# Performance work log

Hardware: AMD Instinct MI355X
Metric: run time of the kernel (lower is better)

## Reference

```python
import jax, jax.numpy as jnp
import numpy as np

N, C, NUM_ELL, E = 1024, 128, 16, 10          # nodes, channels, sum(2l+1) for lmax=3, num_elements
OUT_IRREPS = [(0, 1), (1, 3)]                  # (l_out, 2*l_out+1) for target 128x0e + 128x1o
CORRELATION = 3
NPATHS = {3: 11, 2: 4, 1: 1}                   # generalized-CG path counts per correlation order


def setup_inputs() -> dict:
    key = jax.random.key(0)
    ks = jax.random.split(key, 40)
    node_feats = jax.random.normal(ks[0], (N, C, NUM_ELL), dtype=jnp.float32)
    elem = jax.random.randint(ks[1], (N,), 0, E)
    node_attrs = jax.nn.one_hot(elem, E, dtype=jnp.float32)           # one-hot element indicator
    out_dim = C * sum(d for _, d in OUT_IRREPS)                        # 512
    sc = jax.random.normal(ks[2], (N, out_dim), dtype=jnp.float32)
    inp = {"node_feats": node_feats, "sc": sc, "node_attrs": node_attrs}
    i = 3
    for li, (_, d) in enumerate(OUT_IRREPS):
        for nu in range(1, CORRELATION + 1):
            k = NPATHS[nu]
            # U_nu: generalized CG tensor, shape [d_out, num_ell^nu ..., n_paths]
            inp[f"U_{li}_{nu}"] = jax.random.normal(ks[i], (d,) + (NUM_ELL,) * nu + (k,), dtype=jnp.float32) * np.float32(0.1)
            i += 1
            # element-indexed path weights [num_elements, n_paths, channels]
            inp[f"W_{li}_{nu}"] = jax.random.normal(ks[i], (E, k, C), dtype=jnp.float32) * np.float32(1.0 / np.sqrt(k * C))
            i += 1
        # e3nn-style per-irrep linear mixing multiplicities [C, C]
        inp[f"lin_{li}"] = jax.random.normal(ks[i], (C, C), dtype=jnp.float32)
        i += 1
    return inp


def _sym_contraction(x, y, U, W):
    # x: [N, C, num_ell], y: [N, E]; MACE Contraction recursion (highest order first)
    nu = CORRELATION
    wb = jnp.einsum("ekc,be->bkc", W[nu], y)                 # gather per-element weights
    out = jnp.einsum("...ik,bkc,bci->bc...", U[nu], wb, x)   # [N, C, d, ell, ell] for nu=3
    for nu in range(CORRELATION - 1, 0, -1):
        wb = jnp.einsum("ekc,be->bkc", W[nu], y)
        c = jnp.einsum("...k,bkc->bc...", U[nu], wb) + out
        out = jnp.einsum("bc...i,bci->bc...", c, x)          # contract one ell axis per step
    return out                                               # [N, C, d_out]


def reference(node_feats, sc, node_attrs,
              U_0_1, U_0_2, U_0_3, W_0_1, W_0_2, W_0_3, lin_0,
              U_1_1, U_1_2, U_1_3, W_1_1, W_1_2, W_1_3, lin_1):
    Us = [{1: U_0_1, 2: U_0_2, 3: U_0_3}, {1: U_1_1, 2: U_1_2, 3: U_1_3}]
    Ws = [{1: W_0_1, 2: W_0_2, 3: W_0_3}, {1: W_1_1, 2: W_1_2, 3: W_1_3}]
    lins = [lin_0, lin_1]
    inv_sqrt_c = np.float32(1.0 / np.sqrt(C))                # e3nn Linear fan-in normalization
    blocks = []
    for li in range(len(OUT_IRREPS)):
        feats = _sym_contraction(node_feats, node_attrs, Us[li], Ws[li])   # [N, C, d]
        lin_out = jnp.einsum("bcd,cf->bfd", feats, lins[li]) * inv_sqrt_c
        blocks.append(lin_out.reshape(node_feats.shape[0], -1))           # mul_ir flatten [N, C*d]
    return jnp.concatenate(blocks, axis=-1) + sc             # residual self-connection
```

## Files before the change

### kernel.cpp

```cpp
#include <hip/hip_runtime.h>

#define N_NODES 1024
#define C_CH    128
#define N_ELEM  10
#define K3      11
#define W3PM    1040
#define SU2OFF  49920

__global__ __launch_bounds__(256) void precompute_kernel(
    const float* __restrict__ U03, const float* __restrict__ U02,
    const float* __restrict__ U13, const float* __restrict__ U12,
    float* __restrict__ ws)
{
  const int t = blockIdx.x * 256 + threadIdx.x;
  if (t < 4160) {
    const int m = t / W3PM;
    const int j = t - m * W3PM;
    int a = 0, b = 0, off = 0;
    bool fnd = false;
    for (a = 0; a < 16 && !fnd; ++a) {
      for (b = 0; b <= a; ++b) {
        const int rl = ((b >> 2) + 1) << 2;
        if (j < off + rl) { fnd = true; break; }
        off += rl;
      }
      if (fnd) break;
    }
    const int cc = j - off;
    float out[12];
    #pragma unroll
    for (int k = 0; k < 12; ++k) out[k] = 0.f;
    if (cc <= b) {
      const float* U3 = (m == 0) ? U03 : (U13 + (size_t)(m - 1) * 45056);
      int bases[6]; int np = 0;
      if (a == b && b == cc) {
        bases[np++] = ((a * 16 + a) * 16 + a) * K3;
      } else if (a == b) {
        bases[np++] = ((a * 16 + a) * 16 + cc) * K3;
        bases[np++] = ((a * 16 + cc) * 16 + a) * K3;
        bases[np++] = ((cc * 16 + a) * 16 + a) * K3;
      } else if (b == cc) {
        bases[np++] = ((a * 16 + b) * 16 + b) * K3;
        bases[np++] = ((b * 16 + a) * 16 + b) * K3;
        bases[np++] = ((b * 16 + b) * 16 + a) * K3;
      } else {
        bases[np++] = ((a * 16 + b) * 16 + cc) * K3;
        bases[np++] = ((a * 16 + cc) * 16 + b) * K3;
        bases[np++] = ((b * 16 + a) * 16 + cc) * K3;
        bases[np++] = ((b * 16 + cc) * 16 + a) * K3;
        bases[np++] = ((cc * 16 + a) * 16 + b) * K3;
        bases[np++] = ((cc * 16 + b) * 16 + a) * K3;
      }
      for (int p = 0; p < np; ++p) {
        const float* src = U3 + bases[p];
        #pragma unroll
        for (int k = 0; k < K3; ++k) out[k] += src[k];
      }
    }
    float* dst = ws + (size_t)t * 12;
    *(float4*)&dst[0] = make_float4(out[0], out[1], out[2],  out[3]);
    *(float4*)&dst[4] = make_float4(out[4], out[5], out[6],  out[7]);
    *(float4*)&dst[8] = make_float4(out[8], out[9], out[10], out[11]);
  } else if (t < 4704) {
    const int u = t - 4160;
    const int m = u / 136;
    const int q = u - m * 136;
    int a = 0, b = q;
    while (b > a) { b -= (a + 1); ++a; }
    const float* U2 = (m == 0) ? U02 : (U12 + (size_t)(m - 1) * 1024);
    const float* p1 = U2 + (a * 16 + b) * 4;
    float4 r = make_float4(p1[0], p1[1], p1[2], p1[3]);
    if (a != b) {
      const float* p2 = U2 + (b * 16 + a) * 4;
      r.x += p2[0]; r.y += p2[1]; r.z += p2[2]; r.w += p2[3];
    }
    ((float4*)(ws + SU2OFF))[u] = r;
  }
}

__global__ __launch_bounds__(256) void sym_contract_kernel(
    const float* __restrict__ node_feats,
    const float* __restrict__ node_attrs,
    const float* __restrict__ W03, const float* __restrict__ W02,
    const float* __restrict__ W01, const float* __restrict__ W13,
    const float* __restrict__ W12, const float* __restrict__ W11,
    const float* __restrict__ U01, const float* __restrict__ U11,
    const float* __restrict__ ws,
    float* __restrict__ feats_out)
{
  __shared__ float W3c[4 * W3PM];
  __shared__ float T2c[4 * 136];
  __shared__ float T1s[64];
  __shared__ unsigned short nodelist[N_NODES];
  __shared__ float wrow[32];
  __shared__ int cnt;

  const int e   = blockIdx.x / C_CH;
  const int c   = blockIdx.x % C_CH;
  const int tid = threadIdx.x;

  if (tid == 0) cnt = 0;
  if (tid < 32) {
    float v;
    if (tid < 11)       v = W03[(e * K3 + tid) * C_CH + c];
    else if (tid < 15)  v = W02[(e * 4 + (tid - 11)) * C_CH + c];
    else if (tid == 15) v = W01[e * C_CH + c];
    else if (tid < 27)  v = W13[(e * K3 + (tid - 16)) * C_CH + c];
    else if (tid < 31)  v = W12[(e * 4 + (tid - 27)) * C_CH + c];
    else                v = W11[e * C_CH + c];
    wrow[tid] = v;
  }
  __syncthreads();

  for (int nd = tid; nd < N_NODES; nd += 256)
    if (node_attrs[nd * N_ELEM + e] > 0.5f)
      nodelist[atomicAdd(&cnt, 1)] = (unsigned short)nd;

  for (int ms = 0; ms < 4; ++ms) {
    const int wb = (ms == 0) ? 0 : 16;
    const float w0 = wrow[wb],     w1 = wrow[wb + 1], w2 = wrow[wb + 2];
    const float w3 = wrow[wb + 3], w4 = wrow[wb + 4], w5 = wrow[wb + 5];
    const float w6 = wrow[wb + 6], w7 = wrow[wb + 7], w8 = wrow[wb + 8];
    const float w9 = wrow[wb + 9], wA = wrow[wb + 10];
    for (int j = tid; j < W3PM; j += 256) {
      const float* r = ws + ((size_t)ms * W3PM + j) * 12;
      const float4 r0 = *(const float4*)&r[0];
      const float4 r1 = *(const float4*)&r[4];
      const float4 r2 = *(const float4*)&r[8];
      float acc =       r0.x * w0;
      acc = fmaf(r0.y, w1, acc); acc = fmaf(r0.z, w2, acc);
      acc = fmaf(r0.w, w3, acc); acc = fmaf(r1.x, w4, acc);
      acc = fmaf(r1.y, w5, acc); acc = fmaf(r1.z, w6, acc);
      acc = fmaf(r1.w, w7, acc); acc = fmaf(r2.x, w8, acc);
      acc = fmaf(r2.y, w9, acc); acc = fmaf(r2.z, wA, acc);
      W3c[ms * W3PM + j] = acc;
    }
  }
  const float4* SU2 = (const float4*)(ws + SU2OFF);
  for (int ms = 0; ms < 4; ++ms) {
    const int wb = (ms == 0) ? 11 : 27;
    const float q0 = wrow[wb], q1 = wrow[wb + 1], q2 = wrow[wb + 2], q3 = wrow[wb + 3];
    for (int q = tid; q < 136; q += 256) {
      const float4 r = SU2[ms * 136 + q];
      float acc = r.x * q0;
      acc = fmaf(r.y, q1, acc); acc = fmaf(r.z, q2, acc); acc = fmaf(r.w, q3, acc);
      T2c[ms * 136 + q] = acc;
    }
  }
  if (tid < 64) {
    const int mm = tid >> 4, i1 = tid & 15;
    T1s[tid] = (mm == 0) ? U01[i1] * wrow[15] : U11[(mm - 1) * 16 + i1] * wrow[31];
  }
  __syncthreads();

  const int m    = tid >> 6;
  const int lane = tid & 63;
  const float* W3m = W3c + m * W3PM;
  const float* T2m = T2c + m * 136;
  const float* T1m = T1s + m * 16;
  const int total = cnt;

  for (int base = 0; base < total; base += 64) {
    const int idx     = base + lane;
    const bool active = idx < total;
    const int nd = nodelist[active ? idx : 0];
    const float* xr = node_feats + ((size_t)nd * C_CH + c) * 16;
    float xs[16];
    *(float4*)&xs[0]  = ((const float4*)xr)[0];
    *(float4*)&xs[4]  = ((const float4*)xr)[1];
    *(float4*)&xs[8]  = ((const float4*)xr)[2];
    *(float4*)&xs[12] = ((const float4*)xr)[3];

    float acc0 = 0.f, acc1 = 0.f;
    int woff = 0, tp = 0;
    #pragma unroll
    for (int a = 0; a < 16; ++a) {
      float i1a = T1m[a], i1b = 0.f;
      #pragma unroll
      for (int b = 0; b <= a; ++b) {
        float in2 = T2m[tp];
        #pragma unroll
        for (int q = 0; q <= (b >> 2); ++q) {
          const float4 w4 = *(const float4*)&W3m[woff + 4 * q];
          in2 = fmaf(w4.x, xs[4 * q + 0], in2);
          in2 = fmaf(w4.y, xs[4 * q + 1], in2);
          in2 = fmaf(w4.z, xs[4 * q + 2], in2);
          in2 = fmaf(w4.w, xs[4 * q + 3], in2);
        }
        if (b & 1) i1b = fmaf(in2, xs[b], i1b);
        else       i1a = fmaf(in2, xs[b], i1a);
        woff += ((b >> 2) + 1) << 2;
        ++tp;
      }
      const float in1 = i1a + i1b;
      if (a & 1) acc1 = fmaf(in1, xs[a], acc1);
      else       acc0 = fmaf(in1, xs[a], acc0);
    }
    if (active)
      feats_out[(size_t)nd * 512 + c * 4 + m] = acc0 + acc1;
  }
}

__global__ __launch_bounds__(256) void linear_kernel(
    const float* __restrict__ sc,
    const float* __restrict__ lin0,
    const float* __restrict__ lin1,
    float* __restrict__ io)
{
  __shared__ float f[512];
  const int b   = blockIdx.x;
  const int tid = threadIdx.x;
  const float* row = io + (size_t)b * 512;
  if (tid < 128) ((float4*)f)[tid] = ((const float4*)row)[tid];
  __syncthreads();
  const float inv_sqrt_c = 0.088388347648318447f;
  #pragma unroll
  for (int rep = 0; rep < 2; ++rep) {
    const int o = tid + rep * 256;
    float acc = 0.f;
    if (o < 128) {
      const int fo = o;
      #pragma unroll 4
      for (int ci = 0; ci < 128; ++ci) acc = fmaf(f[ci * 4], lin0[ci * 128 + fo], acc);
    } else {
      const int oo = o - 128;
      const int fo = oo / 3;
      const int dd = oo - fo * 3;
      #pragma unroll 4
      for (int ci = 0; ci < 128; ++ci) acc = fmaf(f[ci * 4 + 1 + dd], lin1[ci * 128 + fo], acc);
    }
    io[(size_t)b * 512 + o] = fmaf(acc, inv_sqrt_c, sc[(size_t)b * 512 + o]);
  }
}

extern "C" void kernel_launch(void* const* d_in, const int* in_sizes, int n_in,
                              void* d_out, int out_size, void* d_ws, size_t ws_size,
                              hipStream_t stream) {
  const float* node_feats = (const float*)d_in[0];
  const float* sc         = (const float*)d_in[1];
  const float* node_attrs = (const float*)d_in[2];
  const float* U01  = (const float*)d_in[3];
  const float* W01  = (const float*)d_in[4];
  const float* U02  = (const float*)d_in[5];
  const float* W02  = (const float*)d_in[6];
  const float* U03  = (const float*)d_in[7];
  const float* W03  = (const float*)d_in[8];
  const float* lin0 = (const float*)d_in[9];
  const float* U11  = (const float*)d_in[10];
  const float* W11  = (const float*)d_in[11];
  const float* U12  = (const float*)d_in[12];
  const float* W12  = (const float*)d_in[13];
  const float* U13  = (const float*)d_in[14];
  const float* W13  = (const float*)d_in[15];
  const float* lin1 = (const float*)d_in[16];
  float* out = (float*)d_out;
  float* ws  = (float*)d_ws;

  precompute_kernel<<<19, 256, 0, stream>>>(U03, U02, U13, U12, ws);
  sym_contract_kernel<<<N_ELEM * C_CH, 256, 0, stream>>>(
      node_feats, node_attrs,
      W03, W02, W01, W13, W12, W11, U01, U11, ws, out);
  linear_kernel<<<N_NODES, 256, 0, stream>>>(sc, lin0, lin1, out);
}
```

Before: 142.1 us.

## Split per-(element,channel) weight table build into separate kernel read from global

Moves the per-block construction of the contracted U·W tables out of the contraction kernel into a dedicated table kernel that writes them to a workspace in global memory. The contraction kernel then reads weights straight from global (uniform scalar loads via readfirstlane) instead of shared memory, which drops the large shared allocation and may raise occupancy. The cost is an extra kernel launch plus about 24 MB of table writes and reads. The path only runs if the workspace is large enough, otherwise it falls back to the old kernel.

```diff
diff --git a/kernel.cpp b/kernel.cpp
--- a/kernel.cpp
+++ b/kernel.cpp
@@ -6,6 +6,8 @@
 #define K3      11
 #define W3PM    1040
 #define SU2OFF  49920
+#define TABOFF  52096
+#define TABSTR  4800
 
 __global__ __launch_bounds__(256) void precompute_kernel(
     const float* __restrict__ U03, const float* __restrict__ U02,
@@ -78,6 +80,146 @@
   }
 }
 
+__device__ __forceinline__ void build_wrow(
+    int e, int c, int tid, float* wrow,
+    const float* W03, const float* W02, const float* W01,
+    const float* W13, const float* W12, const float* W11)
+{
+  if (tid < 32) {
+    float v;
+    if (tid < 11)       v = W03[(e * K3 + tid) * C_CH + c];
+    else if (tid < 15)  v = W02[(e * 4 + (tid - 11)) * C_CH + c];
+    else if (tid == 15) v = W01[e * C_CH + c];
+    else if (tid < 27)  v = W13[(e * K3 + (tid - 16)) * C_CH + c];
+    else if (tid < 31)  v = W12[(e * 4 + (tid - 27)) * C_CH + c];
+    else                v = W11[e * C_CH + c];
+    wrow[tid] = v;
+  }
+}
+
+__global__ __launch_bounds__(256) void table_kernel(
+    const float* __restrict__ ws_su,
+    const float* __restrict__ W03, const float* __restrict__ W02,
+    const float* __restrict__ W01, const float* __restrict__ W13,
+    const float* __restrict__ W12, const float* __restrict__ W11,
+    const float* __restrict__ U01, const float* __restrict__ U11,
+    float* __restrict__ tab)
+{
+  __shared__ float wrow[32];
+  const int bid = blockIdx.x;
+  const int e   = bid / C_CH;
+  const int c   = bid % C_CH;
+  const int tid = threadIdx.x;
+  build_wrow(e, c, tid, wrow, W03, W02, W01, W13, W12, W11);
+  __syncthreads();
+
+  float* Tb = tab + (size_t)bid * TABSTR;
+  for (int ms = 0; ms < 4; ++ms) {
+    const int wb = (ms == 0) ? 0 : 16;
+    const float w0 = wrow[wb],     w1 = wrow[wb + 1], w2 = wrow[wb + 2];
+    const float w3 = wrow[wb + 3], w4 = wrow[wb + 4], w5 = wrow[wb + 5];
+    const float w6 = wrow[wb + 6], w7 = wrow[wb + 7], w8 = wrow[wb + 8];
+    const float w9 = wrow[wb + 9], wA = wrow[wb + 10];
+    for (int j = tid; j < W3PM; j += 256) {
+      const float* r = ws_su + ((size_t)ms * W3PM + j) * 12;
+      const float4 r0 = *(const float4*)&r[0];
+      const float4 r1 = *(const float4*)&r[4];
+      const float4 r2 = *(const float4*)&r[8];
+      float acc =       r0.x * w0;
+      acc = fmaf(r0.y, w1, acc); acc = fmaf(r0.z, w2, acc);
+      acc = fmaf(r0.w, w3, acc); acc = fmaf(r1.x, w4, acc);
+      acc = fmaf(r1.y, w5, acc); acc = fmaf(r1.z, w6, acc);
+      acc = fmaf(r1.w, w7, acc); acc = fmaf(r2.x, w8, acc);
+      acc = fmaf(r2.y, w9, acc); acc = fmaf(r2.z, wA, acc);
+      Tb[ms * W3PM + j] = acc;
+    }
+  }
+  const float4* SU2 = (const float4*)(ws_su + SU2OFF);
+  for (int u = tid; u < 544; u += 256) {
+    const int ms = u / 136;
+    const int wb = (ms == 0) ? 11 : 27;
+    const float4 r = SU2[u];
+    float acc = r.x * wrow[wb];
+    acc = fmaf(r.y, wrow[wb + 1], acc);
+    acc = fmaf(r.z, wrow[wb + 2], acc);
+    acc = fmaf(r.w, wrow[wb + 3], acc);
+    Tb[4160 + u] = acc;
+  }
+  if (tid < 64) {
+    const int mm = tid >> 4, i1 = tid & 15;
+    Tb[4704 + tid] = (mm == 0) ? U01[i1] * wrow[15]
+                               : U11[(mm - 1) * 16 + i1] * wrow[31];
+  }
+}
+
+__global__ __launch_bounds__(256) void sym_contract_scalar(
+    const float* __restrict__ node_feats,
+    const float* __restrict__ node_attrs,
+    const float* __restrict__ tab,
+    float* __restrict__ feats_out)
+{
+  __shared__ unsigned short nodelist[N_NODES];
+  __shared__ int cnt;
+  const int bid = blockIdx.x;
+  const int e   = bid / C_CH;
+  const int c   = bid % C_CH;
+  const int tid = threadIdx.x;
+  if (tid == 0) cnt = 0;
+  __syncthreads();
+  for (int nd = tid; nd < N_NODES; nd += 256)
+    if (node_attrs[nd * N_ELEM + e] > 0.5f)
+      nodelist[atomicAdd(&cnt, 1)] = (unsigned short)nd;
+  __syncthreads();
+
+  const int m    = __builtin_amdgcn_readfirstlane(tid >> 6);
+  const int lane = tid & 63;
+  const float* __restrict__ Tb  = tab + (size_t)bid * TABSTR;
+  const float* __restrict__ W3m = Tb + m * W3PM;
+  const float* __restrict__ T2m = Tb + 4160 + m * 136;
+  const float* __restrict__ T1m = Tb + 4704 + m * 16;
+  const int total = cnt;
+
+  for (int base = 0; base < total; base += 64) {
+    const int idx     = base + lane;
+    const bool active = idx < total;
+    const int nd = nodelist[active ? idx : 0];
+    const float* xr = node_feats + ((size_t)nd * C_CH + c) * 16;
+    float xs[16];
+    *(float4*)&xs[0]  = ((const float4*)xr)[0];
+    *(float4*)&xs[4]  = ((const float4*)xr)[1];
+    *(float4*)&xs[8]  = ((const float4*)xr)[2];
+    *(float4*)&xs[12] = ((const float4*)xr)[3];
+
+    float acc0 = 0.f, acc1 = 0.f;
+    int woff = 0, tp = 0;
+    #pragma unroll
+    for (int a = 0; a < 16; ++a) {
+      float i0 = T1m[a], i1 = 0.f;
+      #pragma unroll
+      for (int b = 0; b <= a; ++b) {
+        float in2 = T2m[tp];
+        #pragma unroll
+        for (int q = 0; q <= (b >> 2); ++q) {
+          const float4 w4 = *(const float4*)&W3m[woff + 4 * q];
+          in2 = fmaf(w4.x, xs[4 * q + 0], in2);
+          in2 = fmaf(w4.y, xs[4 * q + 1], in2);
+          in2 = fmaf(w4.z, xs[4 * q + 2], in2);
+          in2 = fmaf(w4.w, xs[4 * q + 3], in2);
+        }
+        if (b & 1) i1 = fmaf(in2, xs[b], i1);
+        else       i0 = fmaf(in2, xs[b], i0);
+        woff += ((b >> 2) + 1) << 2;
+        ++tp;
+      }
+      const float in1 = i0 + i1;
+      if (a & 1) acc1 = fmaf(in1, xs[a], acc1);
+      else       acc0 = fmaf(in1, xs[a], acc0);
+    }
+    if (active)
+      feats_out[(size_t)nd * 512 + c * 4 + m] = acc0 + acc1;
+  }
+}
+
 __global__ __launch_bounds__(256) void sym_contract_kernel(
     const float* __restrict__ node_feats,
     const float* __restrict__ node_attrs,
@@ -100,16 +242,7 @@
   const int tid = threadIdx.x;
 
   if (tid == 0) cnt = 0;
-  if (tid < 32) {
-    float v;
-    if (tid < 11)       v = W03[(e * K3 + tid) * C_CH + c];
-    else if (tid < 15)  v = W02[(e * 4 + (tid - 11)) * C_CH + c];
-    else if (tid == 15) v = W01[e * C_CH + c];
-    else if (tid < 27)  v = W13[(e * K3 + (tid - 16)) * C_CH + c];
-    else if (tid < 31)  v = W12[(e * 4 + (tid - 27)) * C_CH + c];
-    else                v = W11[e * C_CH + c];
-    wrow[tid] = v;
-  }
+  build_wrow(e, c, tid, wrow, W03, W02, W01, W13, W12, W11);
   __syncthreads();
 
   for (int nd = tid; nd < N_NODES; nd += 256)
@@ -175,7 +308,7 @@
     int woff = 0, tp = 0;
     #pragma unroll
     for (int a = 0; a < 16; ++a) {
-      float i1a = T1m[a], i1b = 0.f;
+      float i0 = T1m[a], i1 = 0.f;
       #pragma unroll
       for (int b = 0; b <= a; ++b) {
         float in2 = T2m[tp];
@@ -187,12 +320,12 @@
           in2 = fmaf(w4.z, xs[4 * q + 2], in2);
           in2 = fmaf(w4.w, xs[4 * q + 3], in2);
         }
-        if (b & 1) i1b = fmaf(in2, xs[b], i1b);
-        else       i1a = fmaf(in2, xs[b], i1a);
+        if (b & 1) i1 = fmaf(in2, xs[b], i1);
+        else       i0 = fmaf(in2, xs[b], i0);
         woff += ((b >> 2) + 1) << 2;
         ++tp;
       }
-      const float in1 = i1a + i1b;
+      const float in1 = i0 + i1;
       if (a & 1) acc1 = fmaf(in1, xs[a], acc1);
       else       acc0 = fmaf(in1, xs[a], acc0);
     }
@@ -256,9 +389,19 @@
   float* out = (float*)d_out;
   float* ws  = (float*)d_ws;
 
+  const size_t need = ((size_t)TABOFF + (size_t)1280 * TABSTR) * 4;
+
   precompute_kernel<<<19, 256, 0, stream>>>(U03, U02, U13, U12, ws);
-  sym_contract_kernel<<<N_ELEM * C_CH, 256, 0, stream>>>(
-      node_feats, node_attrs,
-      W03, W02, W01, W13, W12, W11, U01, U11, ws, out);
+  if (ws_size >= need) {
+    float* tab = ws + TABOFF;
+    table_kernel<<<N_ELEM * C_CH, 256, 0, stream>>>(
+        ws, W03, W02, W01, W13, W12, W11, U01, U11, tab);
+    sym_contract_scalar<<<N_ELEM * C_CH, 256, 0, stream>>>(
+        node_feats, node_attrs, tab, out);
+  } else {
+    sym_contract_kernel<<<N_ELEM * C_CH, 256, 0, stream>>>(
+        node_feats, node_attrs,
+        W03, W02, W01, W13, W12, W11, U01, U11, ws, out);
+  }
   linear_kernel<<<N_NODES, 256, 0, stream>>>(sc, lin0, lin1, out);
 }
```

New measurement: 162.1 us. 1.14x slower.
